# Kernel optimization log

Measured on AMD Instinct MI355X. Metric: run time of the kernel, lower is better.

## Reference

```python
import jax, jax.numpy as jnp
import numpy as np

IN_F, OUT_F, BATCH = 4096, 11008, 8

def setup_inputs() -> dict:
    key = jax.random.key(0)
    k_x, k_s, k_sg, k_b = jax.random.split(key, 4)
    x = jax.random.normal(k_x, (BATCH, IN_F), dtype=jnp.float32)
    # stored codes in [1, 255] as in QINSCodec.encode (uint8 storage)
    stored = jax.random.randint(k_s, (OUT_F, IN_F), 1, 256, dtype=jnp.int32).astype(jnp.uint8)
    # sign in {-1, +1} (int8 storage)
    sign = (jax.random.randint(k_sg, (OUT_F, IN_F), 0, 2, dtype=jnp.int32) * 2 - 1).astype(jnp.int8)
    log_min = jnp.array([-10.0], dtype=jnp.float32)
    log_max = jnp.array([0.0], dtype=jnp.float32)
    bias = jax.random.normal(k_b, (OUT_F,), dtype=jnp.float32) * 0.02
    return {"x": x, "stored": stored, "sign": sign, "log_min": log_min, "log_max": log_max, "bias": bias}

def _decode(stored, sign, log_min, log_max):
    # QINSCodec.decode: normalized = (255 - stored)/254; w = sign * exp(log_min + normalized*(log_max-log_min))
    normalized = (255.0 - stored.astype(jnp.float32)) / 254.0
    log_w = log_min + normalized * (log_max - log_min)
    return sign.astype(jnp.float32) * jnp.exp(log_w)

def reference(x, stored, sign, log_min, log_max, bias):
    lmin = log_min[0]
    lmax = log_max[0]
    w = _decode(stored, sign, lmin, lmax)            # [OUT_F, IN_F]
    return x @ w.T + bias                            # F.linear(x, w, bias)
```

## Files before the change

kernel.cpp:

```cpp
#include <hip/hip_runtime.h>
#include <stdint.h>

#define IN_F   4096
#define OUT_F  11008
#define BATCH  8
#define RPW    4
#define CHUNK  256
#define NCHUNK (IN_F/CHUNK)
#define NSTREAM (2*RPW + BATCH)

typedef __attribute__((address_space(1))) const uint32_t* gas_t;
typedef __attribute__((address_space(3))) uint32_t* las_t;

#define DMA16(gsrc, ldst) \
    __builtin_amdgcn_global_load_lds((gas_t)(gsrc), (las_t)(ldst), 16, 0, 0)

#define VWAIT(N)                                                             \
    do {                                                                     \
        asm volatile("s_waitcnt vmcnt(" #N ")" ::: "memory");                \
        __builtin_amdgcn_sched_barrier(0);                                   \
    } while (0)
#define SBAR() __builtin_amdgcn_sched_barrier(0)

__device__ __forceinline__ float qins_decode(int code, int sgn, float d0, float d1) {
    const float e = __builtin_amdgcn_exp2f(fmaf((float)code, d1, d0));
    const uint32_t m = ((uint32_t)sgn) & 0x80000000u;
    return __uint_as_float(__float_as_uint(e) ^ m);
}

#define ISSUE(T, K)                                                          \
    do {                                                                     \
        const int _ip = (K) * CHUNK + il;                                    \
        _Pragma("unroll")                                                    \
        for (int r = 0; r < RPW; ++r)                                        \
            DMA16(stored + (o0 + r) * IN_F + _ip, &lds[T][r][0]);            \
        _Pragma("unroll")                                                    \
        for (int r = 0; r < RPW; ++r)                                        \
            DMA16(sign + (o0 + r) * IN_F + _ip, &lds[T][RPW + r][0]);        \
        _Pragma("unroll")                                                    \
        for (int b = 0; b < BATCH; ++b)                                      \
            DMA16((const uint32_t*)x + b * IN_F + _ip,                       \
                  &lds[T][2 * RPW + b][0]);                                  \
    } while (0)

#define COMPUTE(T)                                                           \
    do {                                                                     \
        int4 c[RPW], g[RPW];                                                 \
        _Pragma("unroll")                                                    \
        for (int r = 0; r < RPW; ++r) {                                      \
            c[r] = *reinterpret_cast<const int4*>(&lds[T][r][il]);           \
            g[r] = *reinterpret_cast<const int4*>(&lds[T][RPW + r][il]);     \
        }                                                                    \
        float4 xv[BATCH];                                                    \
        _Pragma("unroll")                                                    \
        for (int b = 0; b < BATCH; ++b)                                      \
            xv[b] = *reinterpret_cast<const float4*>(&lds[T][2 * RPW + b][il]); \
        float w[RPW][4];                                                     \
        _Pragma("unroll")                                                    \
        for (int r = 0; r < RPW; ++r) {                                      \
            w[r][0] = qins_decode(c[r].x, g[r].x, d0, d1);                   \
            w[r][1] = qins_decode(c[r].y, g[r].y, d0, d1);                   \
            w[r][2] = qins_decode(c[r].z, g[r].z, d0, d1);                   \
            w[r][3] = qins_decode(c[r].w, g[r].w, d0, d1);                   \
        }                                                                    \
        _Pragma("unroll")                                                    \
        for (int b = 0; b < BATCH; ++b) {                                    \
            _Pragma("unroll")                                                \
            for (int r = 0; r < RPW; ++r) {                                  \
                float a = acc[r][b];                                         \
                a = fmaf(w[r][0], xv[b].x, a);                               \
                a = fmaf(w[r][1], xv[b].y, a);                               \
                a = fmaf(w[r][2], xv[b].z, a);                               \
                a = fmaf(w[r][3], xv[b].w, a);                               \
                acc[r][b] = a;                                               \
            }                                                                \
        }                                                                    \
    } while (0)

__global__ __launch_bounds__(64, 2)
void qins_linear_kernel(const float* __restrict__ x,
                        const uint32_t* __restrict__ stored,
                        const uint32_t* __restrict__ sign,
                        const float* __restrict__ log_min,
                        const float* __restrict__ log_max,
                        const float* __restrict__ bias,
                        float* __restrict__ out)
{
    __shared__ int lds[2][NSTREAM][CHUNK];

    const int lane = threadIdx.x;
    const int o0   = blockIdx.x * RPW;
    const int il   = lane * 4;

    const float lmin = log_min[0];
    const float lmax = log_max[0];
    const float L2E  = 1.44269504088896340736f;
    const float d1 = -(lmax - lmin) * (L2E / 254.0f);
    const float d0 = (lmin + (lmax - lmin) * (255.0f / 254.0f)) * L2E;

    float acc[RPW][BATCH];
#pragma unroll
    for (int r = 0; r < RPW; ++r)
#pragma unroll
        for (int b = 0; b < BATCH; ++b) acc[r][b] = 0.0f;

    ISSUE(0, 0);
    ISSUE(1, 1);
    SBAR();

#pragma unroll 1
    for (int k = 0; k < NCHUNK - 2; k += 2) {
        VWAIT(16);
        COMPUTE(0);
        SBAR();
        ISSUE(0, k + 2);
        SBAR();
        VWAIT(16);
        COMPUTE(1);
        SBAR();
        ISSUE(1, k + 3);
        SBAR();
    }
    VWAIT(16);
    COMPUTE(0);
    VWAIT(0);
    COMPUTE(1);

#pragma unroll
    for (int r = 0; r < RPW; ++r)
#pragma unroll
        for (int b = 0; b < BATCH; ++b) {
            float v = acc[r][b];
#pragma unroll
            for (int s = 32; s >= 1; s >>= 1)
                v += __shfl_xor(v, s, 64);
            acc[r][b] = v;
        }

    if (lane == 0) {
#pragma unroll
        for (int r = 0; r < RPW; ++r) {
            const float bv = bias[o0 + r];
#pragma unroll
            for (int b = 0; b < BATCH; ++b)
                out[(size_t)b * OUT_F + o0 + r] = acc[r][b] + bv;
        }
    }
}

extern "C" void kernel_launch(void* const* d_in, const int* in_sizes, int n_in,
                              void* d_out, int out_size, void* d_ws, size_t ws_size,
                              hipStream_t stream)
{
    const float*    x      = (const float*)d_in[0];
    const uint32_t* stored = (const uint32_t*)d_in[1];
    const uint32_t* sign   = (const uint32_t*)d_in[2];
    const float*    lmin   = (const float*)d_in[3];
    const float*    lmax   = (const float*)d_in[4];
    const float*    bias   = (const float*)d_in[5];
    float* out = (float*)d_out;

    dim3 grid(OUT_F / RPW), block(64);
    qins_linear_kernel<<<grid, block, 0, stream>>>(x, stored, sign, lmin, lmax, bias, out);
}
```

Baseline: 80.83 us.

## Load activations directly from global memory and halve rows per block

Activations are no longer staged into LDS with async DMA. Each lane now reads its float4 slice of x straight from global memory inside the compute step, so only the stored and sign codes go through the LDS double buffer, and the wait counts are lowered to match. Rows per block drop from 4 to 2, which doubles the grid and shrinks LDS and register use, and the occupancy hint is removed. The aim is less LDS traffic and more parallelism. The cost is that x, which is reused by every block, is now fetched twice as often from cache relative to weight bytes.

```diff
diff --git a/kernel.cpp b/kernel.cpp
--- a/kernel.cpp
+++ b/kernel.cpp
@@ -4,10 +4,9 @@
 #define IN_F   4096
 #define OUT_F  11008
 #define BATCH  8
-#define RPW    4
+#define RPW    2
 #define CHUNK  256
 #define NCHUNK (IN_F/CHUNK)
-#define NSTREAM (2*RPW + BATCH)
 
 typedef __attribute__((address_space(1))) const uint32_t* gas_t;
 typedef __attribute__((address_space(3))) uint32_t* las_t;
@@ -37,13 +36,9 @@
         _Pragma("unroll")                                                    \
         for (int r = 0; r < RPW; ++r)                                        \
             DMA16(sign + (o0 + r) * IN_F + _ip, &lds[T][RPW + r][0]);        \
-        _Pragma("unroll")                                                    \
-        for (int b = 0; b < BATCH; ++b)                                      \
-            DMA16((const uint32_t*)x + b * IN_F + _ip,                       \
-                  &lds[T][2 * RPW + b][0]);                                  \
     } while (0)
 
-#define COMPUTE(T)                                                           \
+#define COMPUTE(T, K)                                                        \
     do {                                                                     \
         int4 c[RPW], g[RPW];                                                 \
         _Pragma("unroll")                                                    \
@@ -51,10 +46,6 @@
             c[r] = *reinterpret_cast<const int4*>(&lds[T][r][il]);           \
             g[r] = *reinterpret_cast<const int4*>(&lds[T][RPW + r][il]);     \
         }                                                                    \
-        float4 xv[BATCH];                                                    \
-        _Pragma("unroll")                                                    \
-        for (int b = 0; b < BATCH; ++b)                                      \
-            xv[b] = *reinterpret_cast<const float4*>(&lds[T][2 * RPW + b][il]); \
         float w[RPW][4];                                                     \
         _Pragma("unroll")                                                    \
         for (int r = 0; r < RPW; ++r) {                                      \
@@ -65,19 +56,21 @@
         }                                                                    \
         _Pragma("unroll")                                                    \
         for (int b = 0; b < BATCH; ++b) {                                    \
+            const float4 t = *reinterpret_cast<const float4*>(               \
+                x + b * IN_F + (K) * CHUNK + il);                            \
             _Pragma("unroll")                                                \
             for (int r = 0; r < RPW; ++r) {                                  \
                 float a = acc[r][b];                                         \
-                a = fmaf(w[r][0], xv[b].x, a);                               \
-                a = fmaf(w[r][1], xv[b].y, a);                               \
-                a = fmaf(w[r][2], xv[b].z, a);                               \
-                a = fmaf(w[r][3], xv[b].w, a);                               \
+                a = fmaf(w[r][0], t.x, a);                                   \
+                a = fmaf(w[r][1], t.y, a);                                   \
+                a = fmaf(w[r][2], t.z, a);                                   \
+                a = fmaf(w[r][3], t.w, a);                                   \
                 acc[r][b] = a;                                               \
             }                                                                \
         }                                                                    \
     } while (0)
 
-__global__ __launch_bounds__(64, 2)
+__global__ __launch_bounds__(64)
 void qins_linear_kernel(const float* __restrict__ x,
                         const uint32_t* __restrict__ stored,
                         const uint32_t* __restrict__ sign,
@@ -86,7 +79,7 @@
                         const float* __restrict__ bias,
                         float* __restrict__ out)
 {
-    __shared__ int lds[2][NSTREAM][CHUNK];
+    __shared__ int lds[2][2 * RPW][CHUNK];
 
     const int lane = threadIdx.x;
     const int o0   = blockIdx.x * RPW;
@@ -110,21 +103,21 @@
 
 #pragma unroll 1
     for (int k = 0; k < NCHUNK - 2; k += 2) {
-        VWAIT(16);
-        COMPUTE(0);
+        VWAIT(4);
+        COMPUTE(0, k);
         SBAR();
         ISSUE(0, k + 2);
         SBAR();
-        VWAIT(16);
-        COMPUTE(1);
+        VWAIT(4);
+        COMPUTE(1, k + 1);
         SBAR();
         ISSUE(1, k + 3);
         SBAR();
     }
-    VWAIT(16);
-    COMPUTE(0);
+    VWAIT(4);
+    COMPUTE(0, NCHUNK - 2);
     VWAIT(0);
-    COMPUTE(1);
+    COMPUTE(1, NCHUNK - 1);
 
 #pragma unroll
     for (int r = 0; r < RPW; ++r)
```

Result: slower. 87.62 us (+8.4%).
